# Kernel tuning notes

Measured on AMD Instinct MI355X. Metric: run time of the kernel, lower is better.

Reference implementation:

```python
import jax, jax.numpy as jnp
import numpy as np

TOP_K = 2


def setup_inputs() -> dict:
    key = jax.random.key(0)
    ks = jax.random.split(key, 5)
    B, S, D, F, E = 2, 2048, 1024, 3584, 8
    scale_in = 1.0 / np.sqrt(D)
    scale_ff = 1.0 / np.sqrt(F)
    return {
        "hidden_states": jax.random.normal(ks[0], (B, S, D), dtype=jnp.float32),
        "gate_w": jax.random.normal(ks[1], (E, D), dtype=jnp.float32) * scale_in,
        "w1": jax.random.normal(ks[2], (E, F, D), dtype=jnp.float32) * scale_in,
        "w3": jax.random.normal(ks[3], (E, F, D), dtype=jnp.float32) * scale_in,
        "w2": jax.random.normal(ks[4], (E, D, F), dtype=jnp.float32) * scale_ff,
    }


def reference(hidden_states, gate_w, w1, w3, w2):
    B, S, D = hidden_states.shape
    E = gate_w.shape[0]
    x = hidden_states.reshape(-1, D)                      # [T, D]
    T = x.shape[0]
    router_logits = x @ gate_w.T                          # [T, E]
    probs = jax.nn.softmax(router_logits.astype(jnp.float32), axis=-1)
    top_w, sel = jax.lax.top_k(probs, TOP_K)              # [T, K]
    top_w = top_w / jnp.sum(top_w, axis=-1, keepdims=True)
    top_w = top_w.astype(x.dtype)
    # per-token per-expert combine weight (scatter top-k weights to dense [T, E])
    w_full = jnp.zeros((T, E), dtype=x.dtype).at[jnp.arange(T)[:, None], sel].add(top_w)
    # Original scales the INPUT by the routing weight before the SwiGLU expert;
    # tokens not routed to expert e have weight 0 -> MLP_e(0) == 0 (no biases),
    # so a dense per-expert pass summed over experts reproduces the gather/scatter exactly.
    out = jnp.zeros_like(x)
    for e in range(E):  # fixed small expert count
        xs = x * w_full[:, e:e + 1]                       # [T, D]
        h = jax.nn.silu(xs @ w1[e].T) * (xs @ w3[e].T)    # [T, F]
        out = out + h @ w2[e].T                           # [T, D]
    return out.reshape(B, S, D), router_logits
```

## Files before the change

### kernel.cpp

```cpp
#include <hip/hip_runtime.h>


#define T_TOK 4096
#define D_DIM 1024
#define F_DIM 3584
#define E_NUM 8
#define N13   (2 * F_DIM)
#define BM 128
#define BN 128
#define BK 32
#define LDK (BK + 8)
#define MAXROWS 9216

typedef __bf16 bf16x8 __attribute__((ext_vector_type(8)));
typedef float  f32x4  __attribute__((ext_vector_type(4)));

__device__ __forceinline__ unsigned f2bf_u(float f) {
    unsigned u = __builtin_bit_cast(unsigned, f);
    return (u + 0x7FFFu + ((u >> 16) & 1u)) >> 16;
}
__device__ __forceinline__ unsigned pack2(float lo, float hi) {
    return f2bf_u(lo) | (f2bf_u(hi) << 16);
}
__device__ __forceinline__ int expert_off(const int* __restrict__ counts, int e) {
    int off = 0;
    for (int i = 0; i < e; i++) off += (counts[i] + BM - 1) & ~(BM - 1);
    return off;
}
__device__ __forceinline__ void load_lds16(const void* g, void* l) {
    __builtin_amdgcn_global_load_lds(
        (const __attribute__((address_space(1))) unsigned*)g,
        (__attribute__((address_space(3))) unsigned*)l, 16, 0, 0);
}

__global__ __launch_bounds__(256)
void router(const float* __restrict__ x, const float* __restrict__ gw,
            float* __restrict__ logits, int* __restrict__ counts,
            int* __restrict__ tok, float* __restrict__ wgt)
{
    const int wave = threadIdx.x >> 6;
    const int lane = threadIdx.x & 63;
    const int t = blockIdx.x * 4 + wave;

    const float* xt = x + (size_t)t * D_DIM + lane * 16;
    float4 xv[4];
#pragma unroll
    for (int i = 0; i < 4; i++) xv[i] = ((const float4*)xt)[i];

    float l[E_NUM];
#pragma unroll
    for (int e = 0; e < E_NUM; e++) {
        const float4* gp = (const float4*)(gw + (size_t)e * D_DIM + lane * 16);
        float d = 0.f;
#pragma unroll
        for (int i = 0; i < 4; i++) {
            float4 g = gp[i];
            d += xv[i].x * g.x + xv[i].y * g.y + xv[i].z * g.z + xv[i].w * g.w;
        }
#pragma unroll
        for (int off = 32; off; off >>= 1) d += __shfl_xor(d, off);
        l[e] = d;
    }
#pragma unroll
    for (int e = 0; e < E_NUM; e++)
        if (lane == e) logits[(size_t)t * E_NUM + e] = l[e];

    int e0 = 0; float v0 = l[0];
#pragma unroll
    for (int e = 1; e < E_NUM; e++) if (l[e] > v0) { v0 = l[e]; e0 = e; }
    int e1 = 0; float v1 = -3.4e38f;
#pragma unroll
    for (int e = 0; e < E_NUM; e++) if (e != e0 && l[e] > v1) { v1 = l[e]; e1 = e; }
    const float p1 = __expf(v1 - v0);
    const float w0 = 1.f / (1.f + p1);
    const float w1 = p1 * w0;

    if (lane < 2) {
        const int   ek = lane ? e1 : e0;
        const float wk = lane ? w1 : w0;
        const int pos = atomicAdd(&counts[ek], 1);
        tok[ek * T_TOK + pos] = (t << 1) | lane;
        wgt[ek * T_TOK + pos] = wk;
    }
}

__global__ __launch_bounds__(256)
void gather(const float* __restrict__ x, const int* __restrict__ counts,
            const int* __restrict__ tok, const float* __restrict__ wgt,
            unsigned short* __restrict__ Xe)
{
    const int e = blockIdx.y;
    const int cnt = counts[e];
    const int cntpad = (cnt + BM - 1) & ~(BM - 1);
    const int r0 = blockIdx.x * BM;
    if (r0 >= cntpad) return;
    const int moff = expert_off(counts, e);

    const int tid = threadIdx.x;
    const int chunk = tid & 63;
    const int rsub = tid >> 6;
#pragma unroll
    for (int i = 0; i < 32; i++) {
        const int r = r0 + rsub + i * 4;
        unsigned short* dst = Xe + (size_t)(moff + r) * D_DIM + chunk * 16;
        uint4 o0 = {0,0,0,0}, o1 = {0,0,0,0};
        if (r < cnt) {
            const int t = tok[e * T_TOK + r] >> 1;
            const float w = wgt[e * T_TOK + r];
            const float4* src = (const float4*)(x + (size_t)t * D_DIM + chunk * 16);
            float4 a = src[0], b = src[1], c = src[2], d = src[3];
            o0.x = pack2(a.x*w, a.y*w); o0.y = pack2(a.z*w, a.w*w);
            o0.z = pack2(b.x*w, b.y*w); o0.w = pack2(b.z*w, b.w*w);
            o1.x = pack2(c.x*w, c.y*w); o1.y = pack2(c.z*w, c.w*w);
            o1.z = pack2(d.x*w, d.y*w); o1.w = pack2(d.z*w, d.w*w);
        }
        ((uint4*)dst)[0] = o0; ((uint4*)dst)[1] = o1;
    }
}

__global__ __launch_bounds__(256)
void conv_w13(const float* __restrict__ w1, const float* __restrict__ w3,
              unsigned short* __restrict__ W13)
{
    const size_t idx = (size_t)blockIdx.x * 256 + threadIdx.x;
    const size_t c = idx * 8;
    const int col = (int)(c & (D_DIM - 1));
    const int r   = (int)(c >> 10);
    const int e   = r / N13;
    const int ng  = r - e * N13;
    const int blk = ng >> 5, rem = ng & 31;
    const float* src = ((rem < 16) ? w1 : w3)
        + ((size_t)e * F_DIM + blk * 16 + (rem & 15)) * D_DIM + col;
    float4 a = ((const float4*)src)[0], b = ((const float4*)src)[1];
    uint4 o;
    o.x = pack2(a.x, a.y); o.y = pack2(a.z, a.w);
    o.z = pack2(b.x, b.y); o.w = pack2(b.z, b.w);
    *(uint4*)(W13 + c) = o;
}

__global__ __launch_bounds__(256)
void conv_w2(const float* __restrict__ w2, unsigned short* __restrict__ W2)
{
    const size_t idx = (size_t)blockIdx.x * 256 + threadIdx.x;
    const size_t c = idx * 8;
    float4 a = ((const float4*)(w2 + c))[0], b = ((const float4*)(w2 + c))[1];
    uint4 o;
    o.x = pack2(a.x, a.y); o.y = pack2(a.z, a.w);
    o.z = pack2(b.x, b.y); o.w = pack2(b.z, b.w);
    *(uint4*)(W2 + c) = o;
}

__global__ __launch_bounds__(256)
void gemm1_bf(const unsigned short* __restrict__ Xe,
              const unsigned short* __restrict__ W13,
              const int* __restrict__ counts, unsigned short* __restrict__ H)
{
    const int e = blockIdx.z;
    const int cnt = counts[e];
    const int m0 = blockIdx.y * BM;
    if (m0 >= cnt) return;
    const int moff = expert_off(counts, e);
    const int n0 = blockIdx.x * BN;

    __shared__ unsigned short As[BM * BK];
    __shared__ unsigned short Bs[BN * BK];

    const int tid = threadIdx.x, lane = tid & 63, wave = tid >> 6;
    const int wm = (wave >> 1) * 64, wn = (wave & 1) * 64;

    const int lrow = lane >> 2, lch = (lane & 3) * 8;
    const unsigned short* gA0 = Xe + (size_t)(moff + m0 + wave * 16 + lrow) * D_DIM + lch;
    const unsigned short* gA1 = gA0 + (size_t)64 * D_DIM;
    const unsigned short* gB0 = W13 + ((size_t)e * N13 + n0 + wave * 16 + lrow) * D_DIM + lch;
    const unsigned short* gB1 = gB0 + (size_t)64 * D_DIM;
    unsigned short* lA0 = &As[(wave * 16) * BK];
    unsigned short* lA1 = &As[(64 + wave * 16) * BK];
    unsigned short* lB0 = &Bs[(wave * 16) * BK];
    unsigned short* lB1 = &Bs[(64 + wave * 16) * BK];

    f32x4 acc[4][4] = {};
    const int ko = (lane >> 4) * 8;
    const int mr = wm + (lane & 15), nr = wn + (lane & 15);

    for (int k0 = 0; k0 < D_DIM; k0 += BK) {
        load_lds16(gA0, lA0); load_lds16(gA1, lA1);
        load_lds16(gB0, lB0); load_lds16(gB1, lB1);
        gA0 += BK; gA1 += BK; gB0 += BK; gB1 += BK;
        __syncthreads();

        bf16x8 af[4], bfm[4];
#pragma unroll
        for (int i = 0; i < 4; i++) {
            af[i]  = *(const bf16x8*)&As[(mr + i * 16) * BK + ko];
            bfm[i] = *(const bf16x8*)&Bs[(nr + i * 16) * BK + ko];
        }
#pragma unroll
        for (int mi = 0; mi < 4; mi++)
#pragma unroll
            for (int ni = 0; ni < 4; ni++)
                acc[mi][ni] = __builtin_amdgcn_mfma_f32_16x16x32_bf16(
                    af[mi], bfm[ni], acc[mi][ni], 0, 0, 0);
        __syncthreads();
    }

    const int fb = ((n0 + wn) >> 1) + (lane & 15);
#pragma unroll
    for (int mi = 0; mi < 4; mi++) {
        const int mrow = moff + m0 + wm + mi * 16 + ((lane >> 4) << 2);
#pragma unroll
        for (int p = 0; p < 2; p++) {
            f32x4 g = acc[mi][2 * p];
            f32x4 u = acc[mi][2 * p + 1];
            const int f = fb + p * 16;
#pragma unroll
            for (int r = 0; r < 4; r++) {
                float gv = g[r];
                float hv = (gv / (1.f + __expf(-gv))) * u[r];
                H[(size_t)(mrow + r) * F_DIM + f] = (unsigned short)f2bf_u(hv);
            }
        }
    }
}

__global__ __launch_bounds__(256)
void gemm2_bf(const unsigned short* __restrict__ H,
              const unsigned short* __restrict__ W2,
              const int* __restrict__ counts, const int* __restrict__ tok,
              float* __restrict__ buf)
{
    const int e = blockIdx.z;
    const int cnt = counts[e];
    const int m0 = blockIdx.y * BM;
    if (m0 >= cnt) return;
    const int moff = expert_off(counts, e);
    const int n0 = blockIdx.x * BN;
    const int* tk = tok + e * T_TOK;

    __shared__ unsigned short As[BM * BK];
    __shared__ unsigned short Bs[BN * BK];

    const int tid = threadIdx.x, lane = tid & 63, wave = tid >> 6;
    const int wm = (wave >> 1) * 64, wn = (wave & 1) * 64;

    const int lrow = lane >> 2, lch = (lane & 3) * 8;
    const unsigned short* gA0 = H + (size_t)(moff + m0 + wave * 16 + lrow) * F_DIM + lch;
    const unsigned short* gA1 = gA0 + (size_t)64 * F_DIM;
    const unsigned short* gB0 = W2 + ((size_t)e * D_DIM + n0 + wave * 16 + lrow) * F_DIM + lch;
    const unsigned short* gB1 = gB0 + (size_t)64 * F_DIM;
    unsigned short* lA0 = &As[(wave * 16) * BK];
    unsigned short* lA1 = &As[(64 + wave * 16) * BK];
    unsigned short* lB0 = &Bs[(wave * 16) * BK];
    unsigned short* lB1 = &Bs[(64 + wave * 16) * BK];

    f32x4 acc[4][4] = {};
    const int ko = (lane >> 4) * 8;
    const int mr = wm + (lane & 15), nr = wn + (lane & 15);

    for (int k0 = 0; k0 < F_DIM; k0 += BK) {
        load_lds16(gA0, lA0); load_lds16(gA1, lA1);
        load_lds16(gB0, lB0); load_lds16(gB1, lB1);
        gA0 += BK; gA1 += BK; gB0 += BK; gB1 += BK;
        __syncthreads();

        bf16x8 af[4], bfm[4];
#pragma unroll
        for (int i = 0; i < 4; i++) {
            af[i]  = *(const bf16x8*)&As[(mr + i * 16) * BK + ko];
            bfm[i] = *(const bf16x8*)&Bs[(nr + i * 16) * BK + ko];
        }
#pragma unroll
        for (int mi = 0; mi < 4; mi++)
#pragma unroll
            for (int ni = 0; ni < 4; ni++)
                acc[mi][ni] = __builtin_amdgcn_mfma_f32_16x16x32_bf16(
                    af[mi], bfm[ni], acc[mi][ni], 0, 0, 0);
        __syncthreads();
    }

#pragma unroll
    for (int mi = 0; mi < 4; mi++) {
        const int mbase = m0 + wm + mi * 16 + ((lane >> 4) << 2);
#pragma unroll
        for (int r = 0; r < 4; r++) {
            const int m = mbase + r;
            if (m < cnt) {
                const int v = tk[m];
                float* orow = buf + ((size_t)(v & 1) * T_TOK + (v >> 1)) * D_DIM
                            + n0 + wn + (lane & 15);
#pragma unroll
                for (int ni = 0; ni < 4; ni++)
                    orow[ni * 16] = acc[mi][ni][r];
            }
        }
    }
}

__global__ __launch_bounds__(256)
void combine(const float* __restrict__ buf, float* __restrict__ out)
{
    const size_t i = (size_t)blockIdx.x * 256 + threadIdx.x;
    float4 a = ((const float4*)buf)[i];
    float4 b = ((const float4*)(buf + (size_t)T_TOK * D_DIM))[i];
    float4 o = {a.x + b.x, a.y + b.y, a.z + b.z, a.w + b.w};
    ((float4*)out)[i] = o;
}

__global__ __launch_bounds__(256)
void legacy_gemm1(const unsigned short* __restrict__ Xe,
                  const float* __restrict__ w1, const float* __restrict__ w3,
                  const int* __restrict__ counts, unsigned short* __restrict__ H)
{
    const int e = blockIdx.z;
    const int cnt = counts[e];
    const int m0 = blockIdx.y * BM;
    if (m0 >= cnt) return;
    const int moff = expert_off(counts, e);
    const int n0 = blockIdx.x * BN;

    const float* W1 = w1 + (size_t)e * F_DIM * D_DIM;
    const float* W3 = w3 + (size_t)e * F_DIM * D_DIM;

    __shared__ unsigned short As[BM * LDK];
    __shared__ unsigned short Bs[BN * LDK];

    const int tid = threadIdx.x;
    const int lane = tid & 63, wave = tid >> 6;
    const int wm = (wave >> 1) * 64, wn = (wave & 1) * 64;
    const int sr = tid >> 1, sc = (tid & 1) * 16;

    const unsigned short* arow = Xe + (size_t)(moff + m0 + sr) * D_DIM + sc;
    const int ng = n0 + sr;
    const int blk = ng >> 5, rem = ng & 31;
    const float* brow = (rem < 16)
        ? (W1 + (size_t)(blk * 16 + rem) * D_DIM + sc)
        : (W3 + (size_t)(blk * 16 + rem - 16) * D_DIM + sc);

    f32x4 acc[4][4] = {};
    const int ko = (lane >> 4) * 8;
    const int mr = wm + (lane & 15);
    const int nr = wn + (lane & 15);

    for (int k0 = 0; k0 < D_DIM; k0 += BK) {
        uint4 a0 = ((const uint4*)(arow + k0))[0];
        uint4 a1 = ((const uint4*)(arow + k0))[1];
        const float4* bp = (const float4*)(brow + k0);
        float4 b0 = bp[0], b1 = bp[1], b2 = bp[2], b3 = bp[3];
        uint4 pb0, pb1;
        pb0.x = pack2(b0.x, b0.y); pb0.y = pack2(b0.z, b0.w);
        pb0.z = pack2(b1.x, b1.y); pb0.w = pack2(b1.z, b1.w);
        pb1.x = pack2(b2.x, b2.y); pb1.y = pack2(b2.z, b2.w);
        pb1.z = pack2(b3.x, b3.y); pb1.w = pack2(b3.z, b3.w);

        __syncthreads();
        ((uint4*)&As[sr * LDK + sc])[0] = a0;
        ((uint4*)&As[sr * LDK + sc])[1] = a1;
        ((uint4*)&Bs[sr * LDK + sc])[0] = pb0;
        ((uint4*)&Bs[sr * LDK + sc])[1] = pb1;
        __syncthreads();

        bf16x8 af[4], bfm[4];
#pragma unroll
        for (int i = 0; i < 4; i++) {
            af[i]  = *(const bf16x8*)&As[(mr + i * 16) * LDK + ko];
            bfm[i] = *(const bf16x8*)&Bs[(nr + i * 16) * LDK + ko];
        }
#pragma unroll
        for (int mi = 0; mi < 4; mi++)
#pragma unroll
            for (int ni = 0; ni < 4; ni++)
                acc[mi][ni] = __builtin_amdgcn_mfma_f32_16x16x32_bf16(
                    af[mi], bfm[ni], acc[mi][ni], 0, 0, 0);
    }

    const int fb = ((n0 + wn) >> 1) + (lane & 15);
#pragma unroll
    for (int mi = 0; mi < 4; mi++) {
        const int mrow = moff + m0 + wm + mi * 16 + ((lane >> 4) << 2);
#pragma unroll
        for (int p = 0; p < 2; p++) {
            f32x4 g = acc[mi][2 * p];
            f32x4 u = acc[mi][2 * p + 1];
            const int f = fb + p * 16;
#pragma unroll
            for (int r = 0; r < 4; r++) {
                float gv = g[r];
                float hv = (gv / (1.f + __expf(-gv))) * u[r];
                H[(size_t)(mrow + r) * F_DIM + f] = (unsigned short)f2bf_u(hv);
            }
        }
    }
}

__global__ __launch_bounds__(256)
void legacy_gemm2(const unsigned short* __restrict__ H, const float* __restrict__ w2,
                  const int* __restrict__ counts, const int* __restrict__ tok,
                  float* __restrict__ out)
{
    const int e = blockIdx.z;
    const int cnt = counts[e];
    const int m0 = blockIdx.y * BM;
    if (m0 >= cnt) return;
    const int moff = expert_off(counts, e);
    const int n0 = blockIdx.x * BN;

    const float* W2 = w2 + (size_t)e * D_DIM * F_DIM;
    const int* tk = tok + e * T_TOK;

    __shared__ unsigned short As[BM * LDK];
    __shared__ unsigned short Bs[BN * LDK];

    const int tid = threadIdx.x;
    const int lane = tid & 63, wave = tid >> 6;
    const int wm = (wave >> 1) * 64, wn = (wave & 1) * 64;
    const int sr = tid >> 1, sc = (tid & 1) * 16;

    const unsigned short* arow = H + (size_t)(moff + m0 + sr) * F_DIM + sc;
    const float* brow = W2 + (size_t)(n0 + sr) * F_DIM + sc;

    f32x4 acc[4][4] = {};
    const int ko = (lane >> 4) * 8;
    const int mr = wm + (lane & 15);
    const int nr = wn + (lane & 15);

    for (int k0 = 0; k0 < F_DIM; k0 += BK) {
        uint4 a0 = ((const uint4*)(arow + k0))[0];
        uint4 a1 = ((const uint4*)(arow + k0))[1];
        const float4* bp = (const float4*)(brow + k0);
        float4 b0 = bp[0], b1 = bp[1], b2 = bp[2], b3 = bp[3];
        uint4 pb0, pb1;
        pb0.x = pack2(b0.x, b0.y); pb0.y = pack2(b0.z, b0.w);
        pb0.z = pack2(b1.x, b1.y); pb0.w = pack2(b1.z, b1.w);
        pb1.x = pack2(b2.x, b2.y); pb1.y = pack2(b2.z, b2.w);
        pb1.z = pack2(b3.x, b3.y); pb1.w = pack2(b3.z, b3.w);

        __syncthreads();
        ((uint4*)&As[sr * LDK + sc])[0] = a0;
        ((uint4*)&As[sr * LDK + sc])[1] = a1;
        ((uint4*)&Bs[sr * LDK + sc])[0] = pb0;
        ((uint4*)&Bs[sr * LDK + sc])[1] = pb1;
        __syncthreads();

        bf16x8 af[4], bfm[4];
#pragma unroll
        for (int i = 0; i < 4; i++) {
            af[i]  = *(const bf16x8*)&As[(mr + i * 16) * LDK + ko];
            bfm[i] = *(const bf16x8*)&Bs[(nr + i * 16) * LDK + ko];
        }
#pragma unroll
        for (int mi = 0; mi < 4; mi++)
#pragma unroll
            for (int ni = 0; ni < 4; ni++)
                acc[mi][ni] = __builtin_amdgcn_mfma_f32_16x16x32_bf16(
                    af[mi], bfm[ni], acc[mi][ni], 0, 0, 0);
    }

#pragma unroll
    for (int mi = 0; mi < 4; mi++) {
        const int mbase = m0 + wm + mi * 16 + ((lane >> 4) << 2);
#pragma unroll
        for (int r = 0; r < 4; r++) {
            const int m = mbase + r;
            if (m < cnt) {
                const int t = tk[m] >> 1;
                float* orow = out + (size_t)t * D_DIM + n0 + wn + (lane & 15);
#pragma unroll
                for (int ni = 0; ni < 4; ni++)
                    atomicAdd(orow + ni * 16, acc[mi][ni][r]);
            }
        }
    }
}

extern "C" void kernel_launch(void* const* d_in, const int* in_sizes, int n_in,
                              void* d_out, int out_size, void* d_ws, size_t ws_size,
                              hipStream_t stream)
{
    const float* x  = (const float*)d_in[0];
    const float* gw = (const float*)d_in[1];
    const float* w1 = (const float*)d_in[2];
    const float* w3 = (const float*)d_in[3];
    const float* w2 = (const float*)d_in[4];
    float* out    = (float*)d_out;
    float* logits = out + (size_t)T_TOK * D_DIM;

    char* ws = (char*)d_ws;
    int*   counts = (int*)ws;
    int*   tok    = (int*)(ws + 256);
    float* wgt    = (float*)(ws + 131328);
    unsigned short* Xe = (unsigned short*)(ws + 262400);
    unsigned short* H  = (unsigned short*)(ws + 19136768);
    float*          buf = (float*)(ws + 85197056);
    unsigned short* W13 = (unsigned short*)(ws + 118751488);
    unsigned short* W2b = (unsigned short*)(ws + 236192000);
    const size_t NEED_FULL = 294912256;

    hipMemsetAsync(counts, 0, E_NUM * sizeof(int), stream);
    router<<<T_TOK / 4, 256, 0, stream>>>(x, gw, logits, counts, tok, wgt);
    gather<<<dim3(T_TOK / BM, E_NUM), 256, 0, stream>>>(x, counts, tok, wgt, Xe);

    if (ws_size >= NEED_FULL) {
        conv_w13<<<(E_NUM * (size_t)N13 * D_DIM / 8) / 256, 256, 0, stream>>>(w1, w3, W13);
        conv_w2<<<(E_NUM * (size_t)D_DIM * F_DIM / 8) / 256, 256, 0, stream>>>(w2, W2b);
        gemm1_bf<<<dim3(N13 / BN, T_TOK / BM, E_NUM), 256, 0, stream>>>(Xe, W13, counts, H);
        gemm2_bf<<<dim3(D_DIM / BN, T_TOK / BM, E_NUM), 256, 0, stream>>>(H, W2b, counts, tok, buf);
        combine<<<(T_TOK * D_DIM / 4) / 256, 256, 0, stream>>>(buf, out);
    } else {
        hipMemsetAsync(out, 0, (size_t)T_TOK * D_DIM * sizeof(float), stream);
        legacy_gemm1<<<dim3(N13 / BN, T_TOK / BM, E_NUM), 256, 0, stream>>>(Xe, w1, w3, counts, H);
        legacy_gemm2<<<dim3(D_DIM / BN, T_TOK / BM, E_NUM), 256, 0, stream>>>(H, w2, counts, tok, out);
    }
}
```

Measured before the change: 770.2 us.

## Split gemm2 along K with atomic accumulation and merge weight conversion kernels

```diff
diff --git a/kernel.cpp b/kernel.cpp
--- a/kernel.cpp
+++ b/kernel.cpp
@@ -9,8 +9,9 @@
 #define BM 128
 #define BN 128
 #define BK 32
+#define KSPL 4
+#define KCH  (F_DIM / KSPL)
 #define LDK (BK + 8)
-#define MAXROWS 9216
 
 typedef __bf16 bf16x8 __attribute__((ext_vector_type(8)));
 typedef float  f32x4  __attribute__((ext_vector_type(4)));
@@ -118,36 +119,37 @@
     }
 }
 
-__global__ __launch_bounds__(256)
-void conv_w13(const float* __restrict__ w1, const float* __restrict__ w3,
-              unsigned short* __restrict__ W13)
-{
-    const size_t idx = (size_t)blockIdx.x * 256 + threadIdx.x;
-    const size_t c = idx * 8;
-    const int col = (int)(c & (D_DIM - 1));
-    const int r   = (int)(c >> 10);
-    const int e   = r / N13;
-    const int ng  = r - e * N13;
-    const int blk = ng >> 5, rem = ng & 31;
-    const float* src = ((rem < 16) ? w1 : w3)
-        + ((size_t)e * F_DIM + blk * 16 + (rem & 15)) * D_DIM + col;
+#define W13_CHUNKS ((size_t)E_NUM * N13 * D_DIM / 8)
+#define W2_CHUNKS  ((size_t)E_NUM * D_DIM * F_DIM / 8)
+
+__global__ __launch_bounds__(256)
+void conv_weights(const float* __restrict__ w1, const float* __restrict__ w3,
+                  const float* __restrict__ w2,
+                  unsigned short* __restrict__ W13, unsigned short* __restrict__ W2b)
+{
+    size_t idx = (size_t)blockIdx.x * 256 + threadIdx.x;
+    const float* src;
+    unsigned short* dst;
+    if (idx < W13_CHUNKS) {
+        const size_t c = idx * 8;
+        const int col = (int)(c & (D_DIM - 1));
+        const int r   = (int)(c >> 10);
+        const int e   = r / N13;
+        const int ng  = r - e * N13;
+        const int blk = ng >> 5, rem = ng & 31;
+        src = ((rem < 16) ? w1 : w3)
+            + ((size_t)e * F_DIM + blk * 16 + (rem & 15)) * D_DIM + col;
+        dst = W13 + c;
+    } else {
+        const size_t c = (idx - W13_CHUNKS) * 8;
+        src = w2 + c;
+        dst = W2b + c;
+    }
     float4 a = ((const float4*)src)[0], b = ((const float4*)src)[1];
     uint4 o;
     o.x = pack2(a.x, a.y); o.y = pack2(a.z, a.w);
     o.z = pack2(b.x, b.y); o.w = pack2(b.z, b.w);
-    *(uint4*)(W13 + c) = o;
-}
-
-__global__ __launch_bounds__(256)
-void conv_w2(const float* __restrict__ w2, unsigned short* __restrict__ W2)
-{
-    const size_t idx = (size_t)blockIdx.x * 256 + threadIdx.x;
-    const size_t c = idx * 8;
-    float4 a = ((const float4*)(w2 + c))[0], b = ((const float4*)(w2 + c))[1];
-    uint4 o;
-    o.x = pack2(a.x, a.y); o.y = pack2(a.z, a.w);
-    o.z = pack2(b.x, b.y); o.w = pack2(b.z, b.w);
-    *(uint4*)(W2 + c) = o;
+    *(uint4*)dst = o;
 }
 
 __global__ __launch_bounds__(256)
@@ -228,13 +230,15 @@
               const int* __restrict__ counts, const int* __restrict__ tok,
               float* __restrict__ buf)
 {
-    const int e = blockIdx.z;
+    const int e  = blockIdx.z >> 2;
+    const int ks = blockIdx.z & (KSPL - 1);
     const int cnt = counts[e];
     const int m0 = blockIdx.y * BM;
     if (m0 >= cnt) return;
     const int moff = expert_off(counts, e);
     const int n0 = blockIdx.x * BN;
     const int* tk = tok + e * T_TOK;
+    const int kbase = ks * KCH;
 
     __shared__ unsigned short As[BM * BK];
     __shared__ unsigned short Bs[BN * BK];
@@ -243,9 +247,9 @@
     const int wm = (wave >> 1) * 64, wn = (wave & 1) * 64;
 
     const int lrow = lane >> 2, lch = (lane & 3) * 8;
-    const unsigned short* gA0 = H + (size_t)(moff + m0 + wave * 16 + lrow) * F_DIM + lch;
+    const unsigned short* gA0 = H + (size_t)(moff + m0 + wave * 16 + lrow) * F_DIM + kbase + lch;
     const unsigned short* gA1 = gA0 + (size_t)64 * F_DIM;
-    const unsigned short* gB0 = W2 + ((size_t)e * D_DIM + n0 + wave * 16 + lrow) * F_DIM + lch;
+    const unsigned short* gB0 = W2 + ((size_t)e * D_DIM + n0 + wave * 16 + lrow) * F_DIM + kbase + lch;
     const unsigned short* gB1 = gB0 + (size_t)64 * F_DIM;
     unsigned short* lA0 = &As[(wave * 16) * BK];
     unsigned short* lA1 = &As[(64 + wave * 16) * BK];
@@ -256,7 +260,7 @@
     const int ko = (lane >> 4) * 8;
     const int mr = wm + (lane & 15), nr = wn + (lane & 15);
 
-    for (int k0 = 0; k0 < F_DIM; k0 += BK) {
+    for (int k0 = 0; k0 < KCH; k0 += BK) {
         load_lds16(gA0, lA0); load_lds16(gA1, lA1);
         load_lds16(gB0, lB0); load_lds16(gB1, lB1);
         gA0 += BK; gA1 += BK; gB0 += BK; gB1 += BK;
@@ -289,7 +293,7 @@
                             + n0 + wn + (lane & 15);
 #pragma unroll
                 for (int ni = 0; ni < 4; ni++)
-                    orow[ni * 16] = acc[mi][ni][r];
+                    atomicAdd(orow + ni * 16, acc[mi][ni][r]);
             }
         }
     }
@@ -499,10 +503,12 @@
     gather<<<dim3(T_TOK / BM, E_NUM), 256, 0, stream>>>(x, counts, tok, wgt, Xe);
 
     if (ws_size >= NEED_FULL) {
-        conv_w13<<<(E_NUM * (size_t)N13 * D_DIM / 8) / 256, 256, 0, stream>>>(w1, w3, W13);
-        conv_w2<<<(E_NUM * (size_t)D_DIM * F_DIM / 8) / 256, 256, 0, stream>>>(w2, W2b);
+        hipMemsetAsync(buf, 0, 2ull * T_TOK * D_DIM * sizeof(float), stream);
+        conv_weights<<<(unsigned)((W13_CHUNKS + W2_CHUNKS) / 256), 256, 0, stream>>>(
+            w1, w3, w2, W13, W2b);
         gemm1_bf<<<dim3(N13 / BN, T_TOK / BM, E_NUM), 256, 0, stream>>>(Xe, W13, counts, H);
-        gemm2_bf<<<dim3(D_DIM / BN, T_TOK / BM, E_NUM), 256, 0, stream>>>(H, W2b, counts, tok, buf);
+        gemm2_bf<<<dim3(D_DIM / BN, T_TOK / BM, E_NUM * KSPL), 256, 0, stream>>>(
+            H, W2b, counts, tok, buf);
         combine<<<(T_TOK * D_DIM / 4) / 256, 256, 0, stream>>>(buf, out);
     } else {
         hipMemsetAsync(out, 0, (size_t)T_TOK * D_DIM * sizeof(float), stream);
```

Result: slower. 794.2 us (+3.1%).
